# Kernel tuning notes

Hardware: AMD Instinct MI355X
Metric: run time of the kernel (lower is better)

The kernel has to match this reference:

```python
import jax, jax.numpy as jnp
import numpy as np

B, P, H, V, E, D = 32, 24, 24, 32000, 300, 512


def setup_inputs() -> dict:
    key = jax.random.key(0)
    ks = jax.random.split(key, 16)
    f32 = jnp.float32

    def nrm(k, shape, fan):
        return jax.random.normal(k, shape, f32) / np.sqrt(fan).astype(np.float32)

    return {
        'premise': jax.random.randint(ks[0], (B, P), 0, V),
        'hypothesis': jax.random.randint(ks[1], (B, H), 0, V),
        'embedding': jax.random.normal(ks[2], (V, E), f32),
        'W_ih': nrm(ks[3], (8 * D, 2 * E), 2 * E),
        'W_hh': nrm(ks[4], (8 * D, 2 * D), 2 * D),
        'b_ih': jnp.zeros((8 * D,), f32),
        'b_hh': jnp.zeros((8 * D,), f32),
        'W_ch': nrm(ks[5], (D, 2 * D), 2 * D),
        'b_ch': jnp.zeros((D,), f32),
        'W_cc': nrm(ks[6], (D, 2 * D), 2 * D),
        'b_cc': jnp.zeros((D,), f32),
        'W1': nrm(ks[7], (D, D), D),
        'b1': jnp.zeros((D,), f32),
        'W2': nrm(ks[8], (D, D), D),
        'b2': jnp.zeros((D,), f32),
        'W3': nrm(ks[9], (3, D), D),
        'b3': jnp.zeros((3,), f32),
    }


def reference(premise, hypothesis, embedding, W_ih, W_hh, b_ih, b_hh,
              W_ch, b_ch, W_cc, b_cc, W1, b1, W2, b2, W3, b3):
    prem = embedding[premise]      # [B,P,E]
    hyp = embedding[hypothesis]    # [B,H,E]
    bsz = prem.shape[0]
    d = W_ch.shape[0]
    prem_t = prem.transpose(1, 0, 2)  # [P,B,E]
    hyp_t = hyp.transpose(1, 0, 2)    # [H,B,E]
    zero = jnp.zeros((bsz, d), prem.dtype)

    def lstm_cell(x, h, c):
        # PyTorch LSTMCell gate order: i, f, g, o
        g = x @ W_ih.T + b_ih + h @ W_hh.T + b_hh
        i, f, gg, o = jnp.split(g, 4, axis=-1)
        c2 = jax.nn.sigmoid(f) * c + jax.nn.sigmoid(i) * jnp.tanh(gg)
        h2 = jax.nn.sigmoid(o) * jnp.tanh(c2)
        return h2, c2

    def outer(row, px):
        # row holds (h,c) of the previous premise row (left neighbors), [H,B,D]
        row_h, row_c = row

        def inner(low, ins):
            lh, lc = low                 # lower neighbor (current row, j-1)
            left_h, left_c, hx = ins     # left neighbor (prev row, j) and hyp emb
            x = jnp.concatenate([px, hx], axis=-1)          # [B,2E]
            hcat = jnp.concatenate([left_h, lh], axis=-1)   # [B,2D]
            ccat = jnp.concatenate([left_c, lc], axis=-1)
            oh, oc = lstm_cell(x, hcat, ccat)
            nh = oh @ W_ch.T + b_ch      # condense to [B,D]
            nc = oc @ W_cc.T + b_cc
            return (nh, nc), (nh, nc)

        _, (nrh, nrc) = jax.lax.scan(inner, (zero, zero), (row_h, row_c, hyp_t))
        return (nrh, nrc), None

    hlen = hyp_t.shape[0]
    init = (jnp.zeros((hlen, bsz, d), prem.dtype),
            jnp.zeros((hlen, bsz, d), prem.dtype))
    (row_h, _), _ = jax.lax.scan(outer, init, prem_t)

    h = row_h[-1]                          # h at grid cell (P,H)
    h = jax.nn.relu(h @ W1.T + b1)
    h = jax.nn.relu(h @ W2.T + b2)
    return jax.nn.softmax(h @ W3.T + b3, axis=1)
```

## Files before the change

kernel.cpp:

```cpp
#include <hip/hip_runtime.h>

#define P_   24
#define H_   24
#define E_   300
#define D_   512
#define TWOD 1024
#define G4   4096
#define SMEMB  27648

typedef __attribute__((ext_vector_type(8))) short bf16x8;
typedef __attribute__((ext_vector_type(4))) float f32x4;

__device__ __forceinline__ float bflo(unsigned w) { return __uint_as_float(w << 16); }
__device__ __forceinline__ float bfhi(unsigned w) { return __uint_as_float(w & 0xffff0000u); }
__device__ __forceinline__ unsigned short f2bf(float f) {
    unsigned int x = __float_as_uint(f);
    unsigned int r = (x + 0x7fffu + ((x >> 16) & 1u)) >> 16;
    return (unsigned short)r;
}
__device__ __forceinline__ float sigf(float x) {
    return 1.0f / (1.0f + __expf(-x));
}
__device__ __forceinline__ float tanh_f(float x) {
    return 2.0f / (1.0f + __expf(-2.0f * x)) - 1.0f;
}

#define CFENCE() asm volatile("" ::: "memory")
#define LD8(p)   __hip_atomic_load((const unsigned long long*)(p), __ATOMIC_RELAXED, __HIP_MEMORY_SCOPE_AGENT)
#define LDF(p)   __hip_atomic_load((const float*)(p), __ATOMIC_RELAXED, __HIP_MEMORY_SCOPE_AGENT)
#define LDU(p)   __hip_atomic_load((const unsigned*)(p), __ATOMIC_RELAXED, __HIP_MEMORY_SCOPE_AGENT)
#define STU(p,v) __hip_atomic_store((unsigned*)(p), (unsigned)(v), __ATOMIC_RELAXED, __HIP_MEMORY_SCOPE_AGENT)
#define STF(p,v) __hip_atomic_store((float*)(p), (float)(v), __ATOMIC_RELAXED, __HIP_MEMORY_SCOPE_AGENT)
#define AADD(p,v) __hip_atomic_fetch_add((unsigned*)(p), (unsigned)(v), __ATOMIC_RELAXED, __HIP_MEMORY_SCOPE_AGENT)

#define OFF_WHHP 0u
#define OFF_WCHB 8388608u
#define OFF_WCCB 9437184u
#define OFF_APRE 10485760u
#define OFF_CPRE 16777216u
#define OFF_PX   23068672u
#define OFF_HX   23560192u
#define OFF_HBB  24051712u
#define OFF_CBF  25624576u
#define OFF_H2B  28770304u
#define OFF_C2B  30343168u
#define OFF_HF   31916032u
#define OFF_T1   33488896u
#define OFF_T2   33554432u
#define OFF_BAR2 33619968u

__global__ __launch_bounds__(256) void k_p0(
        const int* __restrict__ prem, const int* __restrict__ hyp,
        const float* __restrict__ emb, const float* __restrict__ Whh,
        const float* __restrict__ Wch, const float* __restrict__ Wcc,
        char* __restrict__ wsb) {
    unsigned short* WhhP = (unsigned short*)(wsb + OFF_WHHP);
    unsigned short* WchB = (unsigned short*)(wsb + OFF_WCHB);
    unsigned short* WccB = (unsigned short*)(wsb + OFF_WCCB);
    unsigned short* PX   = (unsigned short*)(wsb + OFF_PX);
    unsigned short* HX   = (unsigned short*)(wsb + OFF_HX);

    int gt = blockIdx.x * 256 + threadIdx.x;
    int stride = gridDim.x * 256;
    if (gt < 2560) STU(&((unsigned*)(wsb + OFF_BAR2))[gt], 0u);
    for (int idx = gt; idx < 524288; idx += stride) {
        int n = idx >> 7;
        int k8 = (idx & 127) * 8;
        int q = n >> 10, rest = n & 1023;
        int nt = rest >> 5, u = rest & 31;
        int pr = nt * 128 + q * 32 + u;
        const float* s = Whh + (size_t)n * TWOD + k8;
        float4 va = *(const float4*)s, vb = *(const float4*)(s + 4);
        unsigned short o[8] = {f2bf(va.x), f2bf(va.y), f2bf(va.z), f2bf(va.w),
                               f2bf(vb.x), f2bf(vb.y), f2bf(vb.z), f2bf(vb.w)};
        *(uint4*)(WhhP + (size_t)pr * TWOD + k8) = *(const uint4*)o;
    }
    for (int idx = gt; idx < 131072; idx += stride) {
        int cc = idx & 65535;
        const float* s = ((idx < 65536) ? Wch : Wcc) + (size_t)cc * 8;
        unsigned short* dp = ((idx < 65536) ? WchB : WccB) + (size_t)cc * 8;
        float4 va = *(const float4*)s, vb = *(const float4*)(s + 4);
        unsigned short o[8] = {f2bf(va.x), f2bf(va.y), f2bf(va.z), f2bf(va.w),
                               f2bf(vb.x), f2bf(vb.y), f2bf(vb.z), f2bf(vb.w)};
        *(uint4*)dp = *(const uint4*)o;
    }
    for (int idx = gt; idx < 61440; idx += stride) {
        int isH = idx >= 30720 ? 1 : 0;
        int id2 = idx - isH * 30720;
        int rb = id2 / 40, c8 = (id2 % 40) * 8;
        int ri = rb >> 5, rbb = rb & 31;
        int tok = isH ? hyp[rbb * H_ + ri] : prem[rbb * P_ + ri];
        const float* s = emb + (size_t)tok * E_ + c8;
        unsigned short o[8];
        for (int e = 0; e < 8; ++e)
            o[e] = (c8 + e < E_) ? f2bf(s[e]) : (unsigned short)0;
        *(uint4*)((isH ? HX : PX) + rb * 320 + c8) = *(const uint4*)o;
    }
}

__global__ __launch_bounds__(256) void k_p1(
        const float* __restrict__ Wih, const float* __restrict__ bih,
        const float* __restrict__ bhh, char* __restrict__ wsb) {
    const unsigned short* PX = (const unsigned short*)(wsb + OFF_PX);
    const unsigned short* HX = (const unsigned short*)(wsb + OFF_HX);
    unsigned short* Apre = (unsigned short*)(wsb + OFF_APRE);
    unsigned short* Cpre = (unsigned short*)(wsb + OFF_CPRE);

    __shared__ __align__(16) unsigned char smem[SMEMB];
    const int t = threadIdx.x;
    const int lane = t & 63, wvi = t >> 6, l16 = lane & 15, quad = lane >> 4;
    const int wm = wvi >> 1, wn = wvi & 1;
    unsigned short (*At)[72] = (unsigned short (*)[72])smem;
    unsigned short (*Bt)[72] = (unsigned short (*)[72])(smem + 9216);

    int q = blockIdx.x;
    int x = q & 7, slot = q >> 3;
    int z = slot / 48, rem = slot % 48;
    int ntg = rem / 12, mt = rem % 12;
    int nt = ntg * 8 + x;
    const unsigned short* X = z ? HX : PX;
    int koff = z ? E_ : 0;
    unsigned short* Out = z ? Cpre : Apre;
    f32x4 acc[2][4] = {};
    int arow = t >> 2, acol = (t & 3) * 16;
    int brow = t >> 1, bcol = (t & 1) * 32;
    for (int s = 0; s < 5; ++s) {
        int k0 = s * 64;
        {
            const uint4* src = (const uint4*)(X + (size_t)(mt * 64 + arow) * 320 + k0 + acol);
            uint4* dst = (uint4*)&At[arow][acol];
            dst[0] = src[0]; dst[1] = src[1];
        }
        {
            int n = nt * 128 + brow;
            const float* wrow = Wih + (size_t)n * (2 * E_) + koff;
            unsigned short* dst = &Bt[brow][bcol];
            for (int c4 = 0; c4 < 8; ++c4) {
                int k = k0 + bcol + c4 * 4;
                if (k < E_) {
                    float4 v = *(const float4*)(wrow + k);
                    dst[c4 * 4 + 0] = f2bf(v.x); dst[c4 * 4 + 1] = f2bf(v.y);
                    dst[c4 * 4 + 2] = f2bf(v.z); dst[c4 * 4 + 3] = f2bf(v.w);
                } else {
                    dst[c4 * 4 + 0] = 0; dst[c4 * 4 + 1] = 0;
                    dst[c4 * 4 + 2] = 0; dst[c4 * 4 + 3] = 0;
                }
            }
        }
        __syncthreads();
        for (int ks = 0; ks < 2; ++ks) {
            bf16x8 a[2], bb[4];
            for (int mi = 0; mi < 2; ++mi)
                a[mi] = *(const bf16x8*)&At[wm * 32 + mi * 16 + l16][ks * 32 + quad * 8];
            for (int ni = 0; ni < 4; ++ni)
                bb[ni] = *(const bf16x8*)&Bt[wn * 64 + ni * 16 + l16][ks * 32 + quad * 8];
            for (int mi = 0; mi < 2; ++mi)
                for (int ni = 0; ni < 4; ++ni)
                    acc[mi][ni] = __builtin_amdgcn_mfma_f32_16x16x32_bf16(
                        a[mi], bb[ni], acc[mi][ni], 0, 0, 0);
        }
        __syncthreads();
    }
    for (int mi = 0; mi < 2; ++mi) {
        int rbase = mt * 64 + wm * 32 + mi * 16 + quad * 4;
        for (int ni = 0; ni < 4; ++ni) {
            int n = nt * 128 + wn * 64 + ni * 16 + l16;
            int g = n >> 10, cc = n & 1023;
            int knt = cc >> 5, u = cc & 31;
            float bias = z ? 0.0f : (bih[n] + bhh[n]);
            for (int r = 0; r < 4; ++r) {
                size_t ta = (((size_t)knt * 768 + (rbase + r)) * 4 + g) * 32 + u;
                Out[ta] = f2bf(acc[mi][ni][r] + bias);
            }
        }
    }
}

__device__ __forceinline__ void stageA(
        unsigned char* smem, int t,
        const unsigned short* srcL, const unsigned short* srcR) {
    const int row = t >> 3;
    const int cb8 = (t & 7) * 8;
    const unsigned swz = (unsigned)((row & 7) << 4);
    #pragma unroll
    for (int half = 0; half < 2; ++half) {
        unsigned long long v[16];
        #pragma unroll
        for (int s = 0; s < 8; ++s) {
            int e = cb8 + (half * 8 + s) * 64;
            const unsigned short* src =
                (e < D_) ? (srcL ? srcL + e : nullptr)
                         : (srcR ? srcR + (e - D_) : nullptr);
            if (src) { v[2 * s] = LD8(src); v[2 * s + 1] = LD8(src + 4); }
            else     { v[2 * s] = 0ull;     v[2 * s + 1] = 0ull; }
        }
        #pragma unroll
        for (int s = 0; s < 8; ++s) {
            unsigned e2 = (unsigned)(cb8 + (half * 8 + s) * 64) * 2u;
            unsigned off = (unsigned)row * 2048u + (e2 ^ swz);
            *(unsigned long long*)(smem + off)     = v[2 * s];
            *(unsigned long long*)(smem + off + 8) = v[2 * s + 1];
        }
    }
}

__device__ __forceinline__ void gemm_core(
        const unsigned char* smem, int l16, int quad,
        const unsigned short* wrow0, const unsigned short* wrow1,
        f32x4 acc[2][2]) {
    const unsigned sw = (unsigned)((l16 & 7) << 4);
    const unsigned base0 = (unsigned)l16 * 2048u;
    const unsigned base1 = (unsigned)(16 + l16) * 2048u;
    #pragma unroll
    for (int kk = 0; kk < 32; ++kk) {
        unsigned cbyte = (unsigned)(kk * 64 + quad * 16);
        bf16x8 a0 = *(const bf16x8*)(smem + base0 + (cbyte ^ sw));
        bf16x8 a1 = *(const bf16x8*)(smem + base1 + (cbyte ^ sw));
        bf16x8 b0 = *(const bf16x8*)(wrow0 + kk * 32 + quad * 8);
        bf16x8 b1 = *(const bf16x8*)(wrow1 + kk * 32 + quad * 8);
        acc[0][0] = __builtin_amdgcn_mfma_f32_16x16x32_bf16(a0, b0, acc[0][0], 0, 0, 0);
        acc[0][1] = __builtin_amdgcn_mfma_f32_16x16x32_bf16(a0, b1, acc[0][1], 0, 0, 0);
        acc[1][0] = __builtin_amdgcn_mfma_f32_16x16x32_bf16(a1, b0, acc[1][0], 0, 0, 0);
        acc[1][1] = __builtin_amdgcn_mfma_f32_16x16x32_bf16(a1, b1, acc[1][1], 0, 0, 0);
    }
}

__device__ __forceinline__ void gates_job(
        int d, int ncells, int j_lo, int job,
        char* __restrict__ wsb, unsigned char* smem) {
    const unsigned short* WhhP = (const unsigned short*)(wsb + OFF_WHHP);
    const unsigned short* Apre = (const unsigned short*)(wsb + OFF_APRE);
    const unsigned short* Cpre = (const unsigned short*)(wsb + OFF_CPRE);
    const unsigned short* HbB  = (const unsigned short*)(wsb + OFF_HBB);
    const float*          Cbf  = (const float*)(wsb + OFF_CBF);
    unsigned short* H2B = (unsigned short*)(wsb + OFF_H2B);
    unsigned short* C2B = (unsigned short*)(wsb + OFF_C2B);

    int x = job & 7, slot = job >> 3;
    int ntg = slot / ncells, c = slot - ntg * ncells;
    int nt = ntg * 8 + x;
    int cj = j_lo + c, ci = d - cj;

    const unsigned short* HpB = HbB + (size_t)((d + 1) & 1) * (H_ * 32 * D_);
    const float* Cp = Cbf + (size_t)((d + 1) & 1) * (H_ * 32 * D_);

    const int t = threadIdx.x;
    const int lane = t & 63, wvi = t >> 6, l16 = lane & 15, quad = lane >> 4;

    __syncthreads();
    {
        const int row = t >> 3;
        const unsigned short* srcL =
            (ci > 0) ? HpB + (size_t)(cj * 32 + row) * D_ : nullptr;
        const unsigned short* srcR =
            (cj > 0) ? HpB + (size_t)((cj - 1) * 32 + row) * D_ : nullptr;
        stageA(smem, t, srcL, srcR);
    }
    __syncthreads();

    const unsigned short* wrow0 =
        WhhP + (size_t)(nt * 128 + wvi * 32 + l16) * TWOD;
    const unsigned short* wrow1 = wrow0 + (size_t)16 * TWOD;
    f32x4 acc[2][2] = {};
    gemm_core(smem, l16, quad, wrow0, wrow1, acc);
    __syncthreads();

    float* Dt = (float*)smem;
    for (int mi = 0; mi < 2; ++mi)
        for (int ni = 0; ni < 2; ++ni) {
            int cc2 = wvi * 32 + ni * 16 + l16;
            int rr = mi * 16 + quad * 4;
            for (int r = 0; r < 4; ++r)
                Dt[(rr + r) * 132 + cc2] = acc[mi][ni][r];
        }
    __syncthreads();
    {
        int u2 = (t & 15) * 2, r0 = (t >> 4) * 2;
        int k = nt * 32 + u2;
        for (int r = r0; r < r0 + 2; ++r) {
            size_t abase = (((size_t)nt * 768 + (ci * 32 + r)) * 4) * 32 + u2;
            size_t cbase = (((size_t)nt * 768 + (cj * 32 + r)) * 4) * 32 + u2;
            unsigned ap0 = *(const unsigned*)&Apre[abase];
            unsigned ap1 = *(const unsigned*)&Apre[abase + 32];
            unsigned ap2 = *(const unsigned*)&Apre[abase + 64];
            unsigned ap3 = *(const unsigned*)&Apre[abase + 96];
            unsigned cp0 = *(const unsigned*)&Cpre[cbase];
            unsigned cp1 = *(const unsigned*)&Cpre[cbase + 32];
            unsigned cp2 = *(const unsigned*)&Cpre[cbase + 64];
            unsigned cp3 = *(const unsigned*)&Cpre[cbase + 96];
            float ccat0, ccat1;
            if (k < D_) {
                if (ci > 0) {
                    const float* cp = Cp + (size_t)(cj * 32 + r) * D_ + k;
                    ccat0 = LDF(cp); ccat1 = LDF(cp + 1);
                } else { ccat0 = 0.0f; ccat1 = 0.0f; }
            } else {
                if (cj > 0) {
                    const float* cp = Cp + (size_t)((cj - 1) * 32 + r) * D_ + (k - D_);
                    ccat0 = LDF(cp); ccat1 = LDF(cp + 1);
                } else { ccat0 = 0.0f; ccat1 = 0.0f; }
            }
            float g00 = Dt[r * 132 +      u2]     + bflo(ap0) + bflo(cp0);
            float g01 = Dt[r * 132 +      u2 + 1] + bfhi(ap0) + bfhi(cp0);
            float g10 = Dt[r * 132 + 32 + u2]     + bflo(ap1) + bflo(cp1);
            float g11 = Dt[r * 132 + 32 + u2 + 1] + bfhi(ap1) + bfhi(cp1);
            float g20 = Dt[r * 132 + 64 + u2]     + bflo(ap2) + bflo(cp2);
            float g21 = Dt[r * 132 + 64 + u2 + 1] + bfhi(ap2) + bfhi(cp2);
            float g30 = Dt[r * 132 + 96 + u2]     + bflo(ap3) + bflo(cp3);
            float g31 = Dt[r * 132 + 96 + u2 + 1] + bfhi(ap3) + bfhi(cp3);
            float c20 = sigf(g10) * ccat0 + sigf(g00) * tanh_f(g20);
            float h20 = sigf(g30) * tanh_f(c20);
            float c21 = sigf(g11) * ccat1 + sigf(g01) * tanh_f(g21);
            float h21 = sigf(g31) * tanh_f(c21);
            unsigned hw = (unsigned)f2bf(h20) | ((unsigned)f2bf(h21) << 16);
            unsigned cw = (unsigned)f2bf(c20) | ((unsigned)f2bf(c21) << 16);
            STU(&H2B[(size_t)(c * 32 + r) * TWOD + k], hw);
            STU(&C2B[(size_t)(c * 32 + r) * TWOD + k], cw);
        }
    }
}

__device__ __forceinline__ void cond_job(
        int d, int j_lo, int job,
        const float* __restrict__ bch, const float* __restrict__ bcc,
        char* __restrict__ wsb, unsigned char* smem) {
    const unsigned short* H2B  = (const unsigned short*)(wsb + OFF_H2B);
    const unsigned short* C2B  = (const unsigned short*)(wsb + OFF_C2B);
    const unsigned short* WchB = (const unsigned short*)(wsb + OFF_WCHB);
    const unsigned short* WccB = (const unsigned short*)(wsb + OFF_WCCB);
    unsigned short* HbB = (unsigned short*)(wsb + OFF_HBB);
    float* Cbf = (float*)(wsb + OFF_CBF);
    float* Hf  = (float*)(wsb + OFF_HF);

    int xcd = job & 7, c = job >> 3;
    int z = xcd >> 2, ntile = xcd & 3;
    const unsigned short* Ain = z ? C2B : H2B;
    const unsigned short* W = z ? WccB : WchB;
    int cj = j_lo + c;

    const int t = threadIdx.x;
    const int lane = t & 63, wvi = t >> 6, l16 = lane & 15, quad = lane >> 4;

    unsigned short* HbC = HbB + (size_t)(d & 1) * (H_ * 32 * D_);
    float* CbC = Cbf + (size_t)(d & 1) * (H_ * 32 * D_);

    __syncthreads();
    {
        const int row = t >> 3;
        const unsigned short* src = Ain + (size_t)(c * 32 + row) * TWOD;
        stageA(smem, t, src, src + D_);
    }
    __syncthreads();

    const unsigned short* wrow0 =
        W + (size_t)(ntile * 128 + wvi * 32 + l16) * TWOD;
    const unsigned short* wrow1 = wrow0 + (size_t)16 * TWOD;
    f32x4 acc[2][2] = {};
    gemm_core(smem, l16, quad, wrow0, wrow1, acc);

    for (int mi = 0; mi < 2; ++mi) {
        int rr = mi * 16 + quad * 4;
        for (int ni = 0; ni < 2; ++ni) {
            int n = ntile * 128 + wvi * 32 + ni * 16 + l16;
            float bsv = z ? bcc[n] : bch[n];
            for (int r = 0; r < 4; ++r) {
                int rb = rr + r;
                float val = acc[mi][ni][r] + bsv;
                if (z) {
                    STF(&CbC[(size_t)(cj * 32 + rb) * D_ + n], val);
                } else {
                    float pv = __shfl_xor(val, 1);
                    if ((lane & 1) == 0) {
                        unsigned w2 = (unsigned)f2bf(val) | ((unsigned)f2bf(pv) << 16);
                        STU(&HbC[(size_t)(cj * 32 + rb) * D_ + n], w2);
                    }
                    if (d == P_ + H_ - 2)
                        STF(&Hf[(size_t)(cj * 32 + rb) * D_ + n], val);
                }
            }
        }
    }
}

__device__ __forceinline__ void fc_job(
        const float* __restrict__ hin, const float* __restrict__ W,
        const float* __restrict__ bias, float* __restrict__ outv, int job,
        float* hsh) {
    int t = threadIdx.x;
    int row = job >> 1, cb = (job & 1) * 256;
    const float* h = hin + (size_t)row * D_;
    hsh[t * 2]     = LDF(h + t * 2);
    hsh[t * 2 + 1] = LDF(h + t * 2 + 1);
    __syncthreads();
    int col = cb + t;
    const float* w = W + (size_t)col * D_;
    float accv = bias[col];
    for (int k = 0; k < D_; k += 4) {
        float4 wv4 = *(const float4*)(w + k);
        float4 hv = *(const float4*)(hsh + k);
        accv += hv.x * wv4.x + hv.y * wv4.y + hv.z * wv4.z + hv.w * wv4.w;
    }
    STF(&outv[(size_t)row * D_ + col], fmaxf(accv, 0.0f));
    __syncthreads();
}

__device__ __forceinline__ void sm_job(
        const float* __restrict__ T2, const float* __restrict__ W3,
        const float* __restrict__ b3, float* __restrict__ out, float* lg) {
    int t = threadIdx.x;
    if (t < 96) {
        int rb = t / 3, cls = t % 3;
        const float* h = T2 + (size_t)rb * D_;
        const float* w = W3 + (size_t)cls * D_;
        float accv = b3[cls];
        for (int k = 0; k < D_; k += 4) {
            float4 wv4 = *(const float4*)(w + k);
            accv += LDF(h + k) * wv4.x + LDF(h + k + 1) * wv4.y +
                    LDF(h + k + 2) * wv4.z + LDF(h + k + 3) * wv4.w;
        }
        lg[rb * 3 + cls] = accv;
    }
    __syncthreads();
    if (t < 32) {
        float a = lg[t * 3 + 0], bq = lg[t * 3 + 1], cq = lg[t * 3 + 2];
        float m = fmaxf(a, fmaxf(bq, cq));
        float ea = __expf(a - m), eb = __expf(bq - m), ec = __expf(cq - m);
        float s = 1.0f / (ea + eb + ec);
        out[t * 3 + 0] = ea * s;
        out[t * 3 + 1] = eb * s;
        out[t * 3 + 2] = ec * s;
    }
}

__device__ __forceinline__ void gbar(unsigned* bs, unsigned idx, int grid) {
    __syncthreads();
    if (threadIdx.x == 0) {
        unsigned g = blockIdx.x & 31u;
        unsigned gs = (unsigned)grid >> 5;
        CFENCE();
        unsigned old = AADD(bs + g * 32, 1u);
        CFENCE();
        if (old == (idx + 1u) * gs - 1u) {
            unsigned oc = AADD(bs + 1024, 1u);
            CFENCE();
            if (oc == (idx + 1u) * 32u - 1u) {
                #pragma unroll
                for (unsigned gg = 0; gg < 32; ++gg)
                    STU(bs + 1056 + gg * 32, idx + 1u);
            }
        }
        CFENCE();
        while (LDU(bs + 1056 + g * 32) <= idx)
            __builtin_amdgcn_s_sleep(2);
        CFENCE();
    }
    __syncthreads();
}

__global__ __launch_bounds__(256, 2) void k_loop(
        const float* __restrict__ bch, const float* __restrict__ bcc,
        const float* __restrict__ W1, const float* __restrict__ b1,
        const float* __restrict__ W2, const float* __restrict__ b2,
        const float* __restrict__ W3, const float* __restrict__ b3,
        float* __restrict__ outp, char* __restrict__ wsb) {
    __shared__ __align__(16) unsigned char smem[65536];
    unsigned* bs = (unsigned*)(wsb + OFF_BAR2);
    const int grid = gridDim.x;
    unsigned bidx = 0;
    for (int d = 0; d < P_ + H_ - 1; ++d) {
        int j_lo = (d > P_ - 1) ? d - (P_ - 1) : 0;
        int j_hi = (d < H_ - 1) ? d : H_ - 1;
        int ncells = j_hi - j_lo + 1;
        for (int job = blockIdx.x; job < ncells * 32; job += grid)
            gates_job(d, ncells, j_lo, job, wsb, smem);
        gbar(bs, bidx++, grid);
        for (int job = blockIdx.x; job < ncells * 8; job += grid)
            cond_job(d, j_lo, job, bch, bcc, wsb, smem);
        gbar(bs, bidx++, grid);
    }
    const float* hfin = (const float*)(wsb + OFF_HF) + (size_t)(H_ - 1) * 32 * D_;
    float* T1 = (float*)(wsb + OFF_T1);
    float* T2 = (float*)(wsb + OFF_T2);
    __syncthreads();
    if (blockIdx.x < 64) fc_job(hfin, W1, b1, T1, blockIdx.x, (float*)smem);
    gbar(bs, bidx++, grid);
    if (blockIdx.x < 64) fc_job(T1, W2, b2, T2, blockIdx.x, (float*)smem);
    gbar(bs, bidx++, grid);
    if (blockIdx.x == 0) sm_job(T2, W3, b3, outp, (float*)smem);
}

extern "C" void kernel_launch(void* const* d_in, const int* in_sizes, int n_in,
                              void* d_out, int out_size, void* d_ws, size_t ws_size,
                              hipStream_t stream) {
    (void)in_sizes; (void)n_in; (void)out_size; (void)ws_size;

    const int* prem = (const int*)d_in[0];
    const int* hyp  = (const int*)d_in[1];
    const float* emb = (const float*)d_in[2];
    const float* Wih = (const float*)d_in[3];
    const float* Whh = (const float*)d_in[4];
    const float* bih = (const float*)d_in[5];
    const float* bhh = (const float*)d_in[6];
    const float* Wch = (const float*)d_in[7];
    const float* bch = (const float*)d_in[8];
    const float* Wcc = (const float*)d_in[9];
    const float* bcc = (const float*)d_in[10];
    const float* W1  = (const float*)d_in[11];
    const float* b1  = (const float*)d_in[12];
    const float* W2  = (const float*)d_in[13];
    const float* b2  = (const float*)d_in[14];
    const float* W3  = (const float*)d_in[15];
    const float* b3  = (const float*)d_in[16];
    float* outp = (float*)d_out;
    char* wsb = (char*)d_ws;

    k_p0<<<512, 256, 0, stream>>>(prem, hyp, emb, Whh, Wch, Wcc, wsb);
    k_p1<<<768, 256, 0, stream>>>(Wih, bih, bhh, wsb);
    k_loop<<<512, 256, 0, stream>>>(bch, bcc, W1, b1, W2, b2, W3, b3,
                                    outp, wsb);
}
```

Before: 1.843 ms.

## Stage A operand in two K-halves to halve LDS and raise occupancy

The 32x1024 bf16 A tile is now staged into shared memory in two 512-wide halves with a GEMM pass after each, instead of one full tile. This cuts LDS from 64KB to 32KB, so launch bounds rise to 3 blocks per CU and the persistent grid grows from 512 to 768 blocks. The price is two more block barriers per job and a serialized load-then-compute pattern. The grid-wide barrier also has more participants, which can make each of the many per-diagonal barriers more expensive.

```diff
diff --git a/kernel.cpp b/kernel.cpp
--- a/kernel.cpp
+++ b/kernel.cpp
@@ -176,48 +176,40 @@
     }
 }
 
-__device__ __forceinline__ void stageA(
-        unsigned char* smem, int t,
-        const unsigned short* srcL, const unsigned short* srcR) {
+__device__ __forceinline__ void stageA32(
+        unsigned char* smem, int t, const unsigned short* sp) {
     const int row = t >> 3;
-    const int cb8 = (t & 7) * 8;
+    const int cb = (t & 7) * 8;
     const unsigned swz = (unsigned)((row & 7) << 4);
+    unsigned long long v[16];
     #pragma unroll
-    for (int half = 0; half < 2; ++half) {
-        unsigned long long v[16];
-        #pragma unroll
-        for (int s = 0; s < 8; ++s) {
-            int e = cb8 + (half * 8 + s) * 64;
-            const unsigned short* src =
-                (e < D_) ? (srcL ? srcL + e : nullptr)
-                         : (srcR ? srcR + (e - D_) : nullptr);
-            if (src) { v[2 * s] = LD8(src); v[2 * s + 1] = LD8(src + 4); }
-            else     { v[2 * s] = 0ull;     v[2 * s + 1] = 0ull; }
-        }
-        #pragma unroll
-        for (int s = 0; s < 8; ++s) {
-            unsigned e2 = (unsigned)(cb8 + (half * 8 + s) * 64) * 2u;
-            unsigned off = (unsigned)row * 2048u + (e2 ^ swz);
-            *(unsigned long long*)(smem + off)     = v[2 * s];
-            *(unsigned long long*)(smem + off + 8) = v[2 * s + 1];
-        }
-    }
-}
-
-__device__ __forceinline__ void gemm_core(
+    for (int s = 0; s < 8; ++s) {
+        if (sp) { v[2 * s] = LD8(sp + s * 64); v[2 * s + 1] = LD8(sp + s * 64 + 4); }
+        else    { v[2 * s] = 0ull;             v[2 * s + 1] = 0ull; }
+    }
+    #pragma unroll
+    for (int s = 0; s < 8; ++s) {
+        unsigned e2 = (unsigned)(cb + s * 64) * 2u;
+        unsigned off = (unsigned)row * 1024u + (e2 ^ swz);
+        *(unsigned long long*)(smem + off)     = v[2 * s];
+        *(unsigned long long*)(smem + off + 8) = v[2 * s + 1];
+    }
+}
+
+__device__ __forceinline__ void gemm_half(
         const unsigned char* smem, int l16, int quad,
-        const unsigned short* wrow0, const unsigned short* wrow1,
+        const unsigned short* w0, const unsigned short* w1,
         f32x4 acc[2][2]) {
     const unsigned sw = (unsigned)((l16 & 7) << 4);
-    const unsigned base0 = (unsigned)l16 * 2048u;
-    const unsigned base1 = (unsigned)(16 + l16) * 2048u;
+    const unsigned base0 = (unsigned)l16 * 1024u;
+    const unsigned base1 = (unsigned)(16 + l16) * 1024u;
     #pragma unroll
-    for (int kk = 0; kk < 32; ++kk) {
+    for (int kk = 0; kk < 16; ++kk) {
         unsigned cbyte = (unsigned)(kk * 64 + quad * 16);
         bf16x8 a0 = *(const bf16x8*)(smem + base0 + (cbyte ^ sw));
         bf16x8 a1 = *(const bf16x8*)(smem + base1 + (cbyte ^ sw));
-        bf16x8 b0 = *(const bf16x8*)(wrow0 + kk * 32 + quad * 8);
-        bf16x8 b1 = *(const bf16x8*)(wrow1 + kk * 32 + quad * 8);
+        bf16x8 b0 = *(const bf16x8*)(w0 + kk * 32 + quad * 8);
+        bf16x8 b1 = *(const bf16x8*)(w1 + kk * 32 + quad * 8);
         acc[0][0] = __builtin_amdgcn_mfma_f32_16x16x32_bf16(a0, b0, acc[0][0], 0, 0, 0);
         acc[0][1] = __builtin_amdgcn_mfma_f32_16x16x32_bf16(a0, b1, acc[0][1], 0, 0, 0);
         acc[1][0] = __builtin_amdgcn_mfma_f32_16x16x32_bf16(a1, b0, acc[1][0], 0, 0, 0);
@@ -246,23 +238,23 @@
 
     const int t = threadIdx.x;
     const int lane = t & 63, wvi = t >> 6, l16 = lane & 15, quad = lane >> 4;
-
-    __syncthreads();
-    {
-        const int row = t >> 3;
-        const unsigned short* srcL =
-            (ci > 0) ? HpB + (size_t)(cj * 32 + row) * D_ : nullptr;
-        const unsigned short* srcR =
-            (cj > 0) ? HpB + (size_t)((cj - 1) * 32 + row) * D_ : nullptr;
-        stageA(smem, t, srcL, srcR);
-    }
-    __syncthreads();
+    const int row = t >> 3, cb = (t & 7) * 8;
 
     const unsigned short* wrow0 =
         WhhP + (size_t)(nt * 128 + wvi * 32 + l16) * TWOD;
     const unsigned short* wrow1 = wrow0 + (size_t)16 * TWOD;
     f32x4 acc[2][2] = {};
-    gemm_core(smem, l16, quad, wrow0, wrow1, acc);
+
+    __syncthreads();
+    stageA32(smem, t,
+             (ci > 0) ? HpB + (size_t)(cj * 32 + row) * D_ + cb : nullptr);
+    __syncthreads();
+    gemm_half(smem, l16, quad, wrow0, wrow1, acc);
+    __syncthreads();
+    stageA32(smem, t,
+             (cj > 0) ? HpB + (size_t)((cj - 1) * 32 + row) * D_ + cb : nullptr);
+    __syncthreads();
+    gemm_half(smem, l16, quad, wrow0 + 512, wrow1 + 512, acc);
     __syncthreads();
 
     float* Dt = (float*)smem;
@@ -340,23 +332,25 @@
 
     const int t = threadIdx.x;
     const int lane = t & 63, wvi = t >> 6, l16 = lane & 15, quad = lane >> 4;
+    const int row = t >> 3, cb = (t & 7) * 8;
 
     unsigned short* HbC = HbB + (size_t)(d & 1) * (H_ * 32 * D_);
     float* CbC = Cbf + (size_t)(d & 1) * (H_ * 32 * D_);
-
-    __syncthreads();
-    {
-        const int row = t >> 3;
-        const unsigned short* src = Ain + (size_t)(c * 32 + row) * TWOD;
-        stageA(smem, t, src, src + D_);
-    }
-    __syncthreads();
 
     const unsigned short* wrow0 =
         W + (size_t)(ntile * 128 + wvi * 32 + l16) * TWOD;
     const unsigned short* wrow1 = wrow0 + (size_t)16 * TWOD;
+    const unsigned short* asrc = Ain + (size_t)(c * 32 + row) * TWOD + cb;
     f32x4 acc[2][2] = {};
-    gemm_core(smem, l16, quad, wrow0, wrow1, acc);
+
+    __syncthreads();
+    stageA32(smem, t, asrc);
+    __syncthreads();
+    gemm_half(smem, l16, quad, wrow0, wrow1, acc);
+    __syncthreads();
+    stageA32(smem, t, asrc + 512);
+    __syncthreads();
+    gemm_half(smem, l16, quad, wrow0 + 512, wrow1 + 512, acc);
 
     for (int mi = 0; mi < 2; ++mi) {
         int rr = mi * 16 + quad * 4;
@@ -457,13 +451,13 @@
     __syncthreads();
 }
 
-__global__ __launch_bounds__(256, 2) void k_loop(
+__global__ __launch_bounds__(256, 3) void k_loop(
         const float* __restrict__ bch, const float* __restrict__ bcc,
         const float* __restrict__ W1, const float* __restrict__ b1,
         const float* __restrict__ W2, const float* __restrict__ b2,
         const float* __restrict__ W3, const float* __restrict__ b3,
         float* __restrict__ outp, char* __restrict__ wsb) {
-    __shared__ __align__(16) unsigned char smem[65536];
+    __shared__ __align__(16) unsigned char smem[32768];
     unsigned* bs = (unsigned*)(wsb + OFF_BAR2);
     const int grid = gridDim.x;
     unsigned bidx = 0;
@@ -516,6 +510,6 @@
 
     k_p0<<<512, 256, 0, stream>>>(prem, hyp, emb, Whh, Wch, Wcc, wsb);
     k_p1<<<768, 256, 0, stream>>>(Wih, bih, bhh, wsb);
-    k_loop<<<512, 256, 0, stream>>>(bch, bcc, W1, b1, W2, b2, W3, b3,
+    k_loop<<<768, 256, 0, stream>>>(bch, bcc, W1, b1, W2, b2, W3, b3,
                                     outp, wsb);
 }
```

After: 1.780 ms. 3.4% less time.
